# Kernel optimization log

Measured on AMD Instinct MI355X. Metric: run time of the kernel, lower is better.

The kernel has to match this reference:

```python
import jax, jax.numpy as jnp
import numpy as np

H = 128  # hidden_size


def lstm_layer(x, Wih, Whh, bih, bhh):
    """Unidirectional LSTM layer, batch_first input x: [B, T, I] -> [B, T, H].
    PyTorch gate order: i, f, g, o."""
    B = x.shape[0]
    # precompute input projections as one big GEMM: [B, T, 4H]
    xp = jnp.einsum('bti,gi->btg', x, Wih) + bih + bhh
    xp = jnp.transpose(xp, (1, 0, 2))  # [T, B, 4H]
    h0 = jnp.zeros((B, H), x.dtype)
    c0 = jnp.zeros((B, H), x.dtype)

    def step(carry, xp_t):
        h, c = carry
        gates = xp_t + h @ Whh.T  # [B, 4H]
        i, f, g, o = jnp.split(gates, 4, axis=-1)
        i = jax.nn.sigmoid(i)
        f = jax.nn.sigmoid(f)
        g = jnp.tanh(g)
        o = jax.nn.sigmoid(o)
        c = f * c + i * g
        h = o * jnp.tanh(c)
        return (h, c), h

    (_, _), ys = jax.lax.scan(step, (h0, c0), xp)
    return jnp.transpose(ys, (1, 0, 2))  # [B, T, H]


def setup_inputs() -> dict:
    key = jax.random.key(0)
    ks = jax.random.split(key, 13)
    s = 0.05
    inp = {
        'x': jax.random.normal(ks[0], (8, 1, 102400), jnp.float32),
        'Wih0': jax.random.normal(ks[1], (4 * H, 1), jnp.float32) * s,
        'Whh0': jax.random.normal(ks[2], (4 * H, H), jnp.float32) * s,
        'bih0': jnp.zeros((4 * H,), jnp.float32),
        'bhh0': jnp.zeros((4 * H,), jnp.float32).at[H:2 * H].set(1.0),
        'Wih1': jax.random.normal(ks[3], (4 * H, H), jnp.float32) * s,
        'Whh1': jax.random.normal(ks[4], (4 * H, H), jnp.float32) * s,
        'bih1': jnp.zeros((4 * H,), jnp.float32),
        'bhh1': jnp.zeros((4 * H,), jnp.float32).at[H:2 * H].set(1.0),
        'fcW1': jax.random.normal(ks[5], (H // 2, H), jnp.float32) * s,
        'fcb1': jnp.zeros((H // 2,), jnp.float32),
        'fcW2': jax.random.normal(ks[6], (11, H // 2), jnp.float32) * s,
        'fcb2': jnp.zeros((11,), jnp.float32),
    }
    return inp


def reference(x, Wih0, Whh0, bih0, bhh0, Wih1, Whh1, bih1, bhh1,
              fcW1, fcb1, fcW2, fcb2):
    # x: [B, 1, L] -> [B, L, 1]  (transpose(1, 2))
    x = jnp.transpose(x, (0, 2, 1))
    h1 = lstm_layer(x, Wih0, Whh0, bih0, bhh0)   # [B, T, H]
    h2 = lstm_layer(h1, Wih1, Whh1, bih1, bhh1)  # [B, T, H]
    pooled = jnp.mean(h2, axis=1)                # [B, H]; dropout is identity in eval
    hid = jax.nn.relu(pooled @ fcW1.T + fcb1)    # [B, H//2]
    logits = hid @ fcW2.T + fcb2                 # [B, 11]
    return logits
```

## Files before the change

### kernel.cpp

```cpp
#include <hip/hip_runtime.h>

#define HH 128
#define G4 512
#define TT 102400
#define BB 8
#define SEGP 36

typedef _Float16 v2h __attribute__((ext_vector_type(2)));
typedef _Float16 v8h __attribute__((ext_vector_type(8)));

#if defined(__has_builtin)
#if __has_builtin(__builtin_amdgcn_fdot2)
#define HAVE_FDOT2 1
#endif
#endif
#ifdef HAVE_FDOT2
#define FDOT2(a, b, c) __builtin_amdgcn_fdot2((a), (b), (c), false)
#else
__device__ __forceinline__ float fdot2_fb(v2h a, v2h b, float c) {
    return fmaf((float)a[0], (float)b[0], fmaf((float)a[1], (float)b[1], c));
}
#define FDOT2(a, b, c) fdot2_fb((a), (b), (c))
#endif

template<int CTRL>
__device__ __forceinline__ float dpp_add(float v) {
    int p = __builtin_amdgcn_update_dpp(0, __float_as_int(v), CTRL, 0xF, 0xF, true);
    return v + __int_as_float(p);
}

__device__ __forceinline__ float sig_f(float x) {
    return __builtin_amdgcn_rcpf(1.0f + __expf(-x));
}
__device__ __forceinline__ float tanh_f(float x) {
    return fmaf(2.0f, __builtin_amdgcn_rcpf(1.0f + __expf(-2.0f * x)), -1.0f);
}

__device__ __forceinline__ void dot8h(const v2h w[8][16],
                                      const _Float16* __restrict__ hbuf,
                                      int l, float s[8]) {
    const v8h* h8 = (const v8h*)(hbuf + 32 * l);
    v8h hv[4];
#pragma unroll
    for (int i = 0; i < 4; ++i) hv[i] = h8[i];
    float acc[8];
#pragma unroll
    for (int r = 0; r < 8; ++r) acc[r] = 0.f;
#pragma unroll
    for (int i = 0; i < 16; ++i) {
        v2h hp = (v2h){hv[i >> 2][2 * (i & 3)], hv[i >> 2][2 * (i & 3) + 1]};
#pragma unroll
        for (int r = 0; r < 8; ++r)
            acc[r] = FDOT2(w[r][i], hp, acc[r]);
    }
#pragma unroll
    for (int r = 0; r < 8; ++r) {
        float v = acc[r];
        v = dpp_add<0xB1>(v);
        v = dpp_add<0x4E>(v);
        s[r] = v;
    }
}

__device__ __forceinline__ void load_w4(const float* __restrict__ W,
                                        int q, int l, float4 w[4][8]) {
#pragma unroll
    for (int m = 0; m < 4; ++m) {
        const float4* rp = (const float4*)(W + (size_t)(q + 128 * m) * HH + 32 * l);
#pragma unroll
        for (int r = 0; r < 8; ++r) w[m][r] = rp[r];
    }
}
__device__ __forceinline__ void quad_dot4(const float4 w[4][8],
                                          const float* __restrict__ hseg,
                                          float s[4]) {
    const float4* h4 = (const float4*)hseg;
    float4 a0 = {0,0,0,0}, a1 = {0,0,0,0}, a2 = {0,0,0,0}, a3 = {0,0,0,0};
#pragma unroll
    for (int r = 0; r < 8; ++r) {
        float4 hv = h4[r];
        a0.x = fmaf(hv.x, w[0][r].x, a0.x); a0.y = fmaf(hv.y, w[0][r].y, a0.y);
        a0.z = fmaf(hv.z, w[0][r].z, a0.z); a0.w = fmaf(hv.w, w[0][r].w, a0.w);
        a1.x = fmaf(hv.x, w[1][r].x, a1.x); a1.y = fmaf(hv.y, w[1][r].y, a1.y);
        a1.z = fmaf(hv.z, w[1][r].z, a1.z); a1.w = fmaf(hv.w, w[1][r].w, a1.w);
        a2.x = fmaf(hv.x, w[2][r].x, a2.x); a2.y = fmaf(hv.y, w[2][r].y, a2.y);
        a2.z = fmaf(hv.z, w[2][r].z, a2.z); a2.w = fmaf(hv.w, w[2][r].w, a2.w);
        a3.x = fmaf(hv.x, w[3][r].x, a3.x); a3.y = fmaf(hv.y, w[3][r].y, a3.y);
        a3.z = fmaf(hv.z, w[3][r].z, a3.z); a3.w = fmaf(hv.w, w[3][r].w, a3.w);
    }
    s[0] = (a0.x + a0.y) + (a0.z + a0.w);
    s[1] = (a1.x + a1.y) + (a1.z + a1.w);
    s[2] = (a2.x + a2.y) + (a2.z + a2.w);
    s[3] = (a3.x + a3.y) + (a3.z + a3.w);
#pragma unroll
    for (int m = 0; m < 4; ++m) {
        s[m] = dpp_add<0xB1>(s[m]);
        s[m] = dpp_add<0x4E>(s[m]);
    }
}

__global__ void __launch_bounds__(256, 1)
lstm_slot_kernel(
    const float* __restrict__ x,
    const float* __restrict__ Wih0, const float* __restrict__ Whh0,
    const float* __restrict__ bih0, const float* __restrict__ bhh0,
    const float* __restrict__ Wih1, const float* __restrict__ Whh1,
    const float* __restrict__ bih1, const float* __restrict__ bhh1,
    float* __restrict__ h1s, float* __restrict__ c1s,
    float* __restrict__ h2s, float* __restrict__ c2s,
    double* __restrict__ pooled,
    _Float16* __restrict__ h1ring,
    float* __restrict__ xpring,
    int c, int chunkT, int nchunks)
{
    __shared__ __align__(16) unsigned char smem[2 * 4 * SEGP * 4];
    const int t = threadIdx.x;

    if (blockIdx.x < 16) {
        const bool isA = (blockIdx.x < 8);
        const int cc = isA ? c : (c - 2);
        if (cc < 0 || cc >= nchunks) return;
        const int b = blockIdx.x & 7;
        const int Q = t >> 2;
        const int l = t & 3;
        const int p = l & 1;
        const int myc = 2 * Q + p;
        const bool writer = (l < 2);

        _Float16* hh = (_Float16*)smem;

        v2h w[8][16];
        const float* Wl = isA ? Whh0 : Whh1;
#pragma unroll
        for (int r = 0; r < 8; ++r) {
            int row = 2 * Q + (r & 1) + 128 * (r >> 1);
            const float4* rp = (const float4*)(Wl + (size_t)row * HH + 32 * l);
#pragma unroll
            for (int i = 0; i < 8; ++i) {
                float4 f = rp[i];
                w[r][2 * i]     = (v2h){(_Float16)f.x, (_Float16)f.y};
                w[r][2 * i + 1] = (v2h){(_Float16)f.z, (_Float16)f.w};
            }
        }
        float bias4[4], wih4[4];
#pragma unroll
        for (int m = 0; m < 4; ++m) {
            int r = myc + 128 * m;
            if (isA) { bias4[m] = bih0[r] + bhh0[r]; wih4[m] = Wih0[r]; }
            else     { bias4[m] = 0.f;               wih4[m] = 0.f;     }
        }
        float* hst = isA ? h1s : h2s;
        float* cst = isA ? c1s : c2s;
        float c_reg = cst[b * HH + myc];
        if (t < HH) hh[t] = (_Float16)hst[b * HH + t];

        _Float16* ringp = h1ring + ((size_t)((c & 1) * BB + b)) * (size_t)chunkT * HH;
        const float4* xb4 = (const float4*)(x + (size_t)b * TT + (size_t)cc * chunkT);
        const float4* xpq = (const float4*)(xpring
            + ((size_t)((cc & 1) * BB + b)) * (size_t)chunkT * G4);

        const int nt4 = chunkT >> 2;
        float4 xq = isA ? xb4[0] : (float4){0, 0, 0, 0};
        float4 xc[4];
        if (!isA) {
#pragma unroll
            for (int u = 0; u < 4; ++u) xc[u] = xpq[(size_t)u * HH + myc];
        }
        double pacc = 0.0;
        float h = 0.f;
        __syncthreads();

        for (int t4 = 0; t4 < nt4; ++t4) {
            float4 xqn = {0, 0, 0, 0};
            float4 xn[4];
            if (isA) {
                if (t4 + 1 < nt4) xqn = xb4[t4 + 1];
            } else if (t4 + 1 < nt4) {
#pragma unroll
                for (int u = 0; u < 4; ++u)
                    xn[u] = xpq[(size_t)(t4 * 4 + 4 + u) * HH + myc];
            } else {
#pragma unroll
                for (int u = 0; u < 4; ++u) xn[u] = (float4){0, 0, 0, 0};
            }
#pragma unroll
            for (int u = 0; u < 4; ++u) {
                const int buf = u & 1;
                float s[8];
                dot8h(w, hh + buf * HH, l, s);
                float s0 = p ? s[1] : s[0];
                float s1 = p ? s[3] : s[2];
                float s2 = p ? s[5] : s[4];
                float s3 = p ? s[7] : s[6];
                float i_, f_, g_, o_;
                if (isA) {
                    float xt = (u == 0) ? xq.x : (u == 1) ? xq.y : (u == 2) ? xq.z : xq.w;
                    i_ = sig_f (fmaf(xt, wih4[0], s0 + bias4[0]));
                    f_ = sig_f (fmaf(xt, wih4[1], s1 + bias4[1]));
                    g_ = tanh_f(fmaf(xt, wih4[2], s2 + bias4[2]));
                    o_ = sig_f (fmaf(xt, wih4[3], s3 + bias4[3]));
                } else {
                    i_ = sig_f (s0 + xc[u].x);
                    f_ = sig_f (s1 + xc[u].y);
                    g_ = tanh_f(s2 + xc[u].z);
                    o_ = sig_f (s3 + xc[u].w);
                }
                c_reg = fmaf(f_, c_reg, i_ * g_);
                h = o_ * tanh_f(c_reg);
                _Float16 hhv = (_Float16)h;
                if (writer) {
                    hh[(buf ^ 1) * HH + myc] = hhv;
                    if (isA) ringp[(size_t)(t4 * 4 + u) * HH + myc] = hhv;
                }
                if (!isA) pacc += (double)h;
                __syncthreads();
            }
            xq = xqn;
            if (!isA) {
#pragma unroll
                for (int u = 0; u < 4; ++u) xc[u] = xn[u];
            }
        }
        if (writer) {
            cst[b * HH + myc] = c_reg;
            hst[b * HH + myc] = h;
            if (!isA) pooled[b * HH + myc] += pacc;
        }

    } else {
        const int bc = c - 1;
        if (bc < 0 || bc >= nchunks) return;
        const int ib = blockIdx.x - 16;
        const int bb = ib >> 4;
        const int sl = (ib >> 1) & 7;
        const int qh = (ib & 1) * 64;
        const int q = (t >> 2) + qh;
        const int l = t & 3;
        float* hs = (float*)smem;
        float4 w[4][8];
        load_w4(Wih1, q, l, w);
        float bias4[4];
#pragma unroll
        for (int m = 0; m < 4; ++m) {
            int r = q + 128 * m;
            bias4[m] = bih1[r] + bhh1[r];
        }
        const _Float16* hrp = h1ring
            + ((size_t)((bc & 1) * BB + bb)) * (size_t)chunkT * HH;
        float* xpw = xpring + ((size_t)((bc & 1) * BB + bb)) * (size_t)chunkT * G4;
        if (t < HH)
            hs[(t >> 5) * SEGP + (t & 31)] = (float)hrp[(size_t)sl * HH + t];
        __syncthreads();
        int pb = 0;
        for (int tt = sl; tt < chunkT; tt += 8) {
            int ttn = tt + 8;
            bool pf = (t < HH) && (ttn < chunkT);
            float hn = 0.f;
            if (pf) hn = (float)hrp[(size_t)ttn * HH + t];
            float s[4];
            quad_dot4(w, &hs[pb * 4 * SEGP + l * SEGP], s);
            if (pf) hs[(pb ^ 1) * 4 * SEGP + (t >> 5) * SEGP + (t & 31)] = hn;
            float v0 = s[0] + bias4[0], v1 = s[1] + bias4[1];
            float v2 = s[2] + bias4[2], v3 = s[3] + bias4[3];
            float val = (l == 0) ? v0 : (l == 1) ? v1 : (l == 2) ? v2 : v3;
            xpw[(size_t)tt * G4 + q * 4 + l] = val;
            __syncthreads();
            pb ^= 1;
        }
    }
}

__global__ void head_kernel(const double* __restrict__ pooled,
                            const float* __restrict__ fcW1, const float* __restrict__ fcb1,
                            const float* __restrict__ fcW2, const float* __restrict__ fcb2,
                            float* __restrict__ out)
{
    __shared__ float p_s[HH];
    __shared__ float hid_s[64];
    const int b = blockIdx.x, t = threadIdx.x;
    if (t < HH) p_s[t] = (float)(pooled[b * HH + t] * (1.0 / (double)TT));
    __syncthreads();
    if (t < 64) {
        float acc = fcb1[t];
#pragma unroll 8
        for (int k = 0; k < HH; ++k) acc = fmaf(p_s[k], fcW1[t * HH + k], acc);
        hid_s[t] = fmaxf(acc, 0.f);
    }
    __syncthreads();
    if (t < 11) {
        float acc = fcb2[t];
#pragma unroll
        for (int k = 0; k < 64; ++k) acc = fmaf(hid_s[k], fcW2[t * 64 + k], acc);
        out[b * 11 + t] = acc;
    }
}

extern "C" void kernel_launch(void* const* d_in, const int* in_sizes, int n_in,
                              void* d_out, int out_size, void* d_ws, size_t ws_size,
                              hipStream_t stream)
{
    const float* x    = (const float*)d_in[0];
    const float* Wih0 = (const float*)d_in[1];
    const float* Whh0 = (const float*)d_in[2];
    const float* bih0 = (const float*)d_in[3];
    const float* bhh0 = (const float*)d_in[4];
    const float* Wih1 = (const float*)d_in[5];
    const float* Whh1 = (const float*)d_in[6];
    const float* bih1 = (const float*)d_in[7];
    const float* bhh1 = (const float*)d_in[8];
    const float* fcW1 = (const float*)d_in[9];
    const float* fcb1 = (const float*)d_in[10];
    const float* fcW2 = (const float*)d_in[11];
    const float* fcb2 = (const float*)d_in[12];
    float* out = (float*)d_out;

    char* wsp = (char*)d_ws;
    float*  h1s    = (float*) (wsp + 0);
    float*  c1s    = (float*) (wsp + 4096);
    float*  h2s    = (float*) (wsp + 8192);
    float*  c2s    = (float*) (wsp + 12288);
    double* pooled = (double*)(wsp + 16384);
    const size_t STATE_BYTES = 24576;

    static const int cands[] = {3200, 1600, 800, 400, 160, 80, 40, 8};
    int chunkT = 8;
    for (int i = 0; i < 8; ++i) {
        size_t need = STATE_BYTES + (size_t)36864 * (size_t)cands[i];
        if (need <= ws_size) { chunkT = cands[i]; break; }
    }
    const int nchunks = TT / chunkT;

    _Float16* h1ring = (_Float16*)(wsp + STATE_BYTES);
    float* xpring = (float*)(wsp + STATE_BYTES + (size_t)2 * BB * chunkT * HH * 2);

    hipMemsetAsync(d_ws, 0, STATE_BYTES, stream);

    const int nslots = nchunks + 2;
    for (int c = 0; c < nslots; ++c) {
        lstm_slot_kernel<<<144, 256, 0, stream>>>(
            x, Wih0, Whh0, bih0, bhh0, Wih1, Whh1, bih1, bhh1,
            h1s, c1s, h2s, c2s, pooled, h1ring, xpring,
            c, chunkT, nchunks);
    }
    head_kernel<<<BB, 128, 0, stream>>>(pooled, fcW1, fcb1, fcW2, fcb2, out);
}
```

Before: 65.18 ms.

## Split each recurrent row over 8 lanes with a DPP transpose-reduce and per-lane gates

Blocks grow from 256 to 512 threads so each hidden-row dot product is split across 8 lanes. A butterfly DPP transpose-reduce leaves each lane holding exactly one gate pre-activation, so each lane evaluates one nonlinearity instead of four, and the gates are exchanged with DPP moves. This halves the per-lane weight registers and shortens the serial per-step dot chain on the latency-bound recurrence. The input-projection blocks switch to the same fp16 fdot2 scheme, which replaces fp32 weights with fp16 and cuts that grid to 64 blocks. The costs are more cross-lane DPP traffic, a larger barrier per timestep, and lower precision for the projection GEMM.

```diff
diff --git a/kernel.cpp b/kernel.cpp
--- a/kernel.cpp
+++ b/kernel.cpp
@@ -4,102 +4,80 @@
 #define G4 512
 #define TT 102400
 #define BB 8
-#define SEGP 36
 
 typedef _Float16 v2h __attribute__((ext_vector_type(2)));
-typedef _Float16 v8h __attribute__((ext_vector_type(8)));
-
-#if defined(__has_builtin)
+
 #if __has_builtin(__builtin_amdgcn_fdot2)
-#define HAVE_FDOT2 1
-#endif
-#endif
-#ifdef HAVE_FDOT2
 #define FDOT2(a, b, c) __builtin_amdgcn_fdot2((a), (b), (c), false)
 #else
-__device__ __forceinline__ float fdot2_fb(v2h a, v2h b, float c) {
+static __device__ __forceinline__ float fdot2_fb(v2h a, v2h b, float c) {
     return fmaf((float)a[0], (float)b[0], fmaf((float)a[1], (float)b[1], c));
 }
 #define FDOT2(a, b, c) fdot2_fb((a), (b), (c))
 #endif
 
 template<int CTRL>
-__device__ __forceinline__ float dpp_add(float v) {
-    int p = __builtin_amdgcn_update_dpp(0, __float_as_int(v), CTRL, 0xF, 0xF, true);
-    return v + __int_as_float(p);
-}
-
-__device__ __forceinline__ float sig_f(float x) {
-    return __builtin_amdgcn_rcpf(1.0f + __expf(-x));
-}
+__device__ __forceinline__ float dpp_mov(float v) {
+    return __int_as_float(
+        __builtin_amdgcn_update_dpp(0, __float_as_int(v), CTRL, 0xF, 0xF, true));
+}
+
 __device__ __forceinline__ float tanh_f(float x) {
     return fmaf(2.0f, __builtin_amdgcn_rcpf(1.0f + __expf(-2.0f * x)), -1.0f);
 }
 
-__device__ __forceinline__ void dot8h(const v2h w[8][16],
-                                      const _Float16* __restrict__ hbuf,
-                                      int l, float s[8]) {
-    const v8h* h8 = (const v8h*)(hbuf + 32 * l);
-    v8h hv[4];
-#pragma unroll
-    for (int i = 0; i < 4; ++i) hv[i] = h8[i];
+union HI { int i; v2h h; };
+
+__device__ __forceinline__ float dotred(const v2h w[8][8],
+                                        const _Float16* __restrict__ hsl,
+                                        bool bp1, bool bp2, bool bp3) {
+    const int4* hp4 = (const int4*)hsl;
+    int4 ha = hp4[0], hb = hp4[1];
+    int hp[8] = {ha.x, ha.y, ha.z, ha.w, hb.x, hb.y, hb.z, hb.w};
     float acc[8];
 #pragma unroll
     for (int r = 0; r < 8; ++r) acc[r] = 0.f;
 #pragma unroll
-    for (int i = 0; i < 16; ++i) {
-        v2h hp = (v2h){hv[i >> 2][2 * (i & 3)], hv[i >> 2][2 * (i & 3) + 1]};
-#pragma unroll
-        for (int r = 0; r < 8; ++r)
-            acc[r] = FDOT2(w[r][i], hp, acc[r]);
-    }
+    for (int i = 0; i < 8; ++i) {
+        HI u; u.i = hp[i];
+#pragma unroll
+        for (int r = 0; r < 8; ++r) acc[r] = FDOT2(w[r][i], u.h, acc[r]);
+    }
+    float b0[4];
+#pragma unroll
+    for (int m = 0; m < 4; ++m) {
+        float send = bp1 ? acc[2 * m] : acc[2 * m + 1];
+        float keep = bp1 ? acc[2 * m + 1] : acc[2 * m];
+        b0[m] = keep + dpp_mov<0xB1>(send);
+    }
+    float d0[2];
+#pragma unroll
+    for (int i = 0; i < 2; ++i) {
+        float send = bp2 ? b0[i] : b0[i + 2];
+        float keep = bp2 ? b0[i + 2] : b0[i];
+        d0[i] = keep + dpp_mov<0x4E>(send);
+    }
+    float send = bp3 ? d0[0] : d0[1];
+    float keep = bp3 ? d0[1] : d0[0];
+    return keep + dpp_mov<0x141>(send);
+}
+
+__device__ __forceinline__ void load_w8h(const float* __restrict__ W,
+                                         int Q, int j, v2h w[8][8]) {
 #pragma unroll
     for (int r = 0; r < 8; ++r) {
-        float v = acc[r];
-        v = dpp_add<0xB1>(v);
-        v = dpp_add<0x4E>(v);
-        s[r] = v;
-    }
-}
-
-__device__ __forceinline__ void load_w4(const float* __restrict__ W,
-                                        int q, int l, float4 w[4][8]) {
-#pragma unroll
-    for (int m = 0; m < 4; ++m) {
-        const float4* rp = (const float4*)(W + (size_t)(q + 128 * m) * HH + 32 * l);
-#pragma unroll
-        for (int r = 0; r < 8; ++r) w[m][r] = rp[r];
-    }
-}
-__device__ __forceinline__ void quad_dot4(const float4 w[4][8],
-                                          const float* __restrict__ hseg,
-                                          float s[4]) {
-    const float4* h4 = (const float4*)hseg;
-    float4 a0 = {0,0,0,0}, a1 = {0,0,0,0}, a2 = {0,0,0,0}, a3 = {0,0,0,0};
-#pragma unroll
-    for (int r = 0; r < 8; ++r) {
-        float4 hv = h4[r];
-        a0.x = fmaf(hv.x, w[0][r].x, a0.x); a0.y = fmaf(hv.y, w[0][r].y, a0.y);
-        a0.z = fmaf(hv.z, w[0][r].z, a0.z); a0.w = fmaf(hv.w, w[0][r].w, a0.w);
-        a1.x = fmaf(hv.x, w[1][r].x, a1.x); a1.y = fmaf(hv.y, w[1][r].y, a1.y);
-        a1.z = fmaf(hv.z, w[1][r].z, a1.z); a1.w = fmaf(hv.w, w[1][r].w, a1.w);
-        a2.x = fmaf(hv.x, w[2][r].x, a2.x); a2.y = fmaf(hv.y, w[2][r].y, a2.y);
-        a2.z = fmaf(hv.z, w[2][r].z, a2.z); a2.w = fmaf(hv.w, w[2][r].w, a2.w);
-        a3.x = fmaf(hv.x, w[3][r].x, a3.x); a3.y = fmaf(hv.y, w[3][r].y, a3.y);
-        a3.z = fmaf(hv.z, w[3][r].z, a3.z); a3.w = fmaf(hv.w, w[3][r].w, a3.w);
-    }
-    s[0] = (a0.x + a0.y) + (a0.z + a0.w);
-    s[1] = (a1.x + a1.y) + (a1.z + a1.w);
-    s[2] = (a2.x + a2.y) + (a2.z + a2.w);
-    s[3] = (a3.x + a3.y) + (a3.z + a3.w);
-#pragma unroll
-    for (int m = 0; m < 4; ++m) {
-        s[m] = dpp_add<0xB1>(s[m]);
-        s[m] = dpp_add<0x4E>(s[m]);
-    }
-}
-
-__global__ void __launch_bounds__(256, 1)
+        int row = 2 * Q + (r & 1) + 128 * (r >> 1);
+        const float4* rp = (const float4*)(W + (size_t)row * HH + 16 * j);
+#pragma unroll
+        for (int i = 0; i < 4; ++i) {
+            float4 f = rp[i];
+            w[r][2 * i]     = (v2h){(_Float16)f.x, (_Float16)f.y};
+            w[r][2 * i + 1] = (v2h){(_Float16)f.z, (_Float16)f.w};
+        }
+    }
+}
+
+__global__ void __launch_bounds__(512, 2)
 lstm_slot_kernel(
     const float* __restrict__ x,
     const float* __restrict__ Wih0, const float* __restrict__ Whh0,
@@ -113,42 +91,34 @@
     float* __restrict__ xpring,
     int c, int chunkT, int nchunks)
 {
-    __shared__ __align__(16) unsigned char smem[2 * 4 * SEGP * 4];
+    __shared__ __align__(32) _Float16 hh[2 * HH];
     const int t = threadIdx.x;
+    const int Q = t >> 3;
+    const int j = t & 7;
+    const bool bp1 = ((j ^ (j >> 2)) & 1) != 0;
+    const bool bp2 = ((j ^ (j >> 1)) & 1) != 0;
+    const bool bp3 = ((j >> 2) & 1) != 0;
+    const int cellj = bp1 ? 1 : 0;
+    const int gatej = (bp2 ? 2 : 0) + (bp3 ? 1 : 0);
+    const int myc   = 2 * Q + cellj;
+    const int myrow = myc + 128 * gatej;
+    const bool owner = (gatej == 0);
+    const bool isg = (gatej == 2);
+    const float fe = isg ? -2.f : -1.f;
+    const float fm = isg ?  2.f :  1.f;
+    const float fa = isg ? -1.f :  0.f;
 
     if (blockIdx.x < 16) {
         const bool isA = (blockIdx.x < 8);
         const int cc = isA ? c : (c - 2);
         if (cc < 0 || cc >= nchunks) return;
         const int b = blockIdx.x & 7;
-        const int Q = t >> 2;
-        const int l = t & 3;
-        const int p = l & 1;
-        const int myc = 2 * Q + p;
-        const bool writer = (l < 2);
-
-        _Float16* hh = (_Float16*)smem;
-
-        v2h w[8][16];
-        const float* Wl = isA ? Whh0 : Whh1;
-#pragma unroll
-        for (int r = 0; r < 8; ++r) {
-            int row = 2 * Q + (r & 1) + 128 * (r >> 1);
-            const float4* rp = (const float4*)(Wl + (size_t)row * HH + 32 * l);
-#pragma unroll
-            for (int i = 0; i < 8; ++i) {
-                float4 f = rp[i];
-                w[r][2 * i]     = (v2h){(_Float16)f.x, (_Float16)f.y};
-                w[r][2 * i + 1] = (v2h){(_Float16)f.z, (_Float16)f.w};
-            }
-        }
-        float bias4[4], wih4[4];
-#pragma unroll
-        for (int m = 0; m < 4; ++m) {
-            int r = myc + 128 * m;
-            if (isA) { bias4[m] = bih0[r] + bhh0[r]; wih4[m] = Wih0[r]; }
-            else     { bias4[m] = 0.f;               wih4[m] = 0.f;     }
-        }
+
+        v2h w[8][8];
+        load_w8h(isA ? Whh0 : Whh1, Q, j, w);
+        float bias_l = 0.f, wih_l = 0.f;
+        if (isA) { bias_l = bih0[myrow] + bhh0[myrow]; wih_l = Wih0[myrow]; }
+
         float* hst = isA ? h1s : h2s;
         float* cst = isA ? c1s : c2s;
         float c_reg = cst[b * HH + myc];
@@ -156,74 +126,69 @@
 
         _Float16* ringp = h1ring + ((size_t)((c & 1) * BB + b)) * (size_t)chunkT * HH;
         const float4* xb4 = (const float4*)(x + (size_t)b * TT + (size_t)cc * chunkT);
-        const float4* xpq = (const float4*)(xpring
-            + ((size_t)((cc & 1) * BB + b)) * (size_t)chunkT * G4);
+        const float* xps = xpring
+            + ((size_t)((cc & 1) * BB + b)) * (size_t)chunkT * G4 + 4 * myc + gatej;
 
         const int nt4 = chunkT >> 2;
-        float4 xq = isA ? xb4[0] : (float4){0, 0, 0, 0};
-        float4 xc[4];
-        if (!isA) {
-#pragma unroll
-            for (int u = 0; u < 4; ++u) xc[u] = xpq[(size_t)u * HH + myc];
+        float4 xq = {0, 0, 0, 0};
+        float xpc[4] = {0, 0, 0, 0};
+        if (isA) xq = xb4[0];
+        else {
+#pragma unroll
+            for (int u = 0; u < 4; ++u) xpc[u] = xps[(size_t)u * G4];
         }
         double pacc = 0.0;
-        float h = 0.f;
+        float hfin = 0.f;
         __syncthreads();
 
         for (int t4 = 0; t4 < nt4; ++t4) {
             float4 xqn = {0, 0, 0, 0};
-            float4 xn[4];
+            float xpn[4] = {0, 0, 0, 0};
             if (isA) {
                 if (t4 + 1 < nt4) xqn = xb4[t4 + 1];
             } else if (t4 + 1 < nt4) {
 #pragma unroll
                 for (int u = 0; u < 4; ++u)
-                    xn[u] = xpq[(size_t)(t4 * 4 + 4 + u) * HH + myc];
-            } else {
-#pragma unroll
-                for (int u = 0; u < 4; ++u) xn[u] = (float4){0, 0, 0, 0};
+                    xpn[u] = xps[(size_t)(t4 * 4 + 4 + u) * G4];
             }
 #pragma unroll
             for (int u = 0; u < 4; ++u) {
                 const int buf = u & 1;
-                float s[8];
-                dot8h(w, hh + buf * HH, l, s);
-                float s0 = p ? s[1] : s[0];
-                float s1 = p ? s[3] : s[2];
-                float s2 = p ? s[5] : s[4];
-                float s3 = p ? s[7] : s[6];
-                float i_, f_, g_, o_;
+                float sfin = dotred(w, hh + buf * HH + 16 * j, bp1, bp2, bp3);
+                float pre;
                 if (isA) {
-                    float xt = (u == 0) ? xq.x : (u == 1) ? xq.y : (u == 2) ? xq.z : xq.w;
-                    i_ = sig_f (fmaf(xt, wih4[0], s0 + bias4[0]));
-                    f_ = sig_f (fmaf(xt, wih4[1], s1 + bias4[1]));
-                    g_ = tanh_f(fmaf(xt, wih4[2], s2 + bias4[2]));
-                    o_ = sig_f (fmaf(xt, wih4[3], s3 + bias4[3]));
+                    float xt = (u == 0) ? xq.x : (u == 1) ? xq.y
+                             : (u == 2) ? xq.z : xq.w;
+                    pre = fmaf(xt, wih_l, sfin + bias_l);
                 } else {
-                    i_ = sig_f (s0 + xc[u].x);
-                    f_ = sig_f (s1 + xc[u].y);
-                    g_ = tanh_f(s2 + xc[u].z);
-                    o_ = sig_f (s3 + xc[u].w);
+                    pre = sfin + xpc[u];
                 }
-                c_reg = fmaf(f_, c_reg, i_ * g_);
-                h = o_ * tanh_f(c_reg);
-                _Float16 hhv = (_Float16)h;
-                if (writer) {
-                    hh[(buf ^ 1) * HH + myc] = hhv;
-                    if (isA) ringp[(size_t)(t4 * 4 + u) * HH + myc] = hhv;
+                float e  = __expf(pre * fe);
+                float rr = __builtin_amdgcn_rcpf(1.0f + e);
+                float act = fmaf(fm, rr, fa);
+                float t1 = dpp_mov<0x141>(act);
+                float t2 = dpp_mov<0x4E>(act);
+                float t3 = dpp_mov<0x4E>(t1);
+                c_reg = fmaf(t1, c_reg, act * t2);
+                float th = tanh_f(c_reg);
+                float hv = t3 * th;
+                hfin = hv;
+                if (owner) {
+                    hh[(buf ^ 1) * HH + myc] = (_Float16)hv;
+                    if (isA) ringp[(size_t)(t4 * 4 + u) * HH + myc] = (_Float16)hv;
+                    else     pacc += (double)hv;
                 }
-                if (!isA) pacc += (double)h;
                 __syncthreads();
             }
             xq = xqn;
             if (!isA) {
 #pragma unroll
-                for (int u = 0; u < 4; ++u) xc[u] = xn[u];
+                for (int u = 0; u < 4; ++u) xpc[u] = xpn[u];
             }
         }
-        if (writer) {
+        if (owner) {
             cst[b * HH + myc] = c_reg;
-            hst[b * HH + myc] = h;
+            hst[b * HH + myc] = hfin;
             if (!isA) pooled[b * HH + myc] += pacc;
         }
 
@@ -231,39 +196,25 @@
         const int bc = c - 1;
         if (bc < 0 || bc >= nchunks) return;
         const int ib = blockIdx.x - 16;
-        const int bb = ib >> 4;
-        const int sl = (ib >> 1) & 7;
-        const int qh = (ib & 1) * 64;
-        const int q = (t >> 2) + qh;
-        const int l = t & 3;
-        float* hs = (float*)smem;
-        float4 w[4][8];
-        load_w4(Wih1, q, l, w);
-        float bias4[4];
-#pragma unroll
-        for (int m = 0; m < 4; ++m) {
-            int r = q + 128 * m;
-            bias4[m] = bih1[r] + bhh1[r];
-        }
+        const int bb = ib >> 3;
+        const int sl = ib & 7;
+        v2h w[8][8];
+        load_w8h(Wih1, Q, j, w);
+        const float bias_l = bih1[myrow] + bhh1[myrow];
         const _Float16* hrp = h1ring
             + ((size_t)((bc & 1) * BB + bb)) * (size_t)chunkT * HH;
         float* xpw = xpring + ((size_t)((bc & 1) * BB + bb)) * (size_t)chunkT * G4;
-        if (t < HH)
-            hs[(t >> 5) * SEGP + (t & 31)] = (float)hrp[(size_t)sl * HH + t];
+        if (t < HH) hh[t] = hrp[(size_t)sl * HH + t];
         __syncthreads();
         int pb = 0;
         for (int tt = sl; tt < chunkT; tt += 8) {
             int ttn = tt + 8;
             bool pf = (t < HH) && (ttn < chunkT);
-            float hn = 0.f;
-            if (pf) hn = (float)hrp[(size_t)ttn * HH + t];
-            float s[4];
-            quad_dot4(w, &hs[pb * 4 * SEGP + l * SEGP], s);
-            if (pf) hs[(pb ^ 1) * 4 * SEGP + (t >> 5) * SEGP + (t & 31)] = hn;
-            float v0 = s[0] + bias4[0], v1 = s[1] + bias4[1];
-            float v2 = s[2] + bias4[2], v3 = s[3] + bias4[3];
-            float val = (l == 0) ? v0 : (l == 1) ? v1 : (l == 2) ? v2 : v3;
-            xpw[(size_t)tt * G4 + q * 4 + l] = val;
+            _Float16 hn = (_Float16)0.f;
+            if (pf) hn = hrp[(size_t)ttn * HH + t];
+            float sfin = dotred(w, hh + pb * HH + 16 * j, bp1, bp2, bp3);
+            if (pf) hh[(pb ^ 1) * HH + t] = hn;
+            xpw[(size_t)tt * G4 + 4 * myc + gatej] = sfin + bias_l;
             __syncthreads();
             pb ^= 1;
         }
@@ -337,7 +288,7 @@
 
     const int nslots = nchunks + 2;
     for (int c = 0; c < nslots; ++c) {
-        lstm_slot_kernel<<<144, 256, 0, stream>>>(
+        lstm_slot_kernel<<<80, 512, 0, stream>>>(
             x, Wih0, Whh0, bih0, bhh0, Wih1, Whh1, bih1, bhh1,
             h1s, c1s, h2s, c2s, pooled, h1ring, xpring,
             c, chunkT, nchunks);
```

Result: faster. 62.78 ms (-3.7%).
